# Performance work log

Measured on AMD Instinct MI355X. Metric: run time of the kernel, lower is better.

## Reference

```python
import jax, jax.numpy as jnp
import numpy as np

TEMPERATURE = 1.0
EPS = 1e-8


def setup_inputs() -> dict:
    key = jax.random.key(0)
    k1, k2, k3 = jax.random.split(key, 3)
    B, N = 32768, 32
    scores = jax.random.normal(k1, (B, N), dtype=jnp.float32)
    rankings = jax.random.randint(k2, (B, N), 0, 32, dtype=jnp.int64)
    mask = jax.random.randint(k3, (B, N), 0, 2) > 0
    return {"scores": scores, "rankings": rankings, "mask": mask}


def reference(scores, rankings, mask):
    # scores: [B, N] float, rankings: [B, N] int (0 => unranked), mask: [B, N] bool
    s = scores / TEMPERATURE
    valid = mask & (rankings > 0)                      # [B, N]

    ri = rankings[:, :, None]                          # [B, N, 1]
    rj = rankings[:, None, :]                          # [B, 1, N]
    # i==j implies ri==rj, so (ri != rj) also excludes the diagonal
    pair_valid = (valid[:, :, None] & valid[:, None, :] & (ri != rj))  # [B, N, N]

    p_ij = (ri < rj).astype(s.dtype)                   # target probability
    s_ij = jax.nn.sigmoid(s[:, :, None] - s[:, None, :])
    pair_loss = -p_ij * jnp.log(s_ij + EPS) - (1.0 - p_ij) * jnp.log(1.0 - s_ij + EPS)

    pv = pair_valid.astype(s.dtype)
    per_batch_sum = jnp.sum(pair_loss * pv, axis=(1, 2))     # [B]
    num_pairs = jnp.sum(pv, axis=(1, 2))                     # [B]

    has_pairs = num_pairs > 0
    per_batch_loss = jnp.where(has_pairs, per_batch_sum / jnp.maximum(num_pairs, 1.0), 0.0)
    n_batches = jnp.sum(has_pairs.astype(s.dtype))
    # reduction='mean' over batches that contributed pairs; 0.0 if none
    return jnp.where(n_batches > 0, jnp.sum(per_batch_loss) / jnp.maximum(n_batches, 1.0), 0.0)
```

## Files before the change

kernel.cpp:

```cpp
#include <hip/hip_runtime.h>

__global__ __launch_bounds__(256) void ranknet_partial_kernel(
    const float4* __restrict__ scores4,
    const int4*   __restrict__ rank4,
    const int4*   __restrict__ mask4,
    float2*       __restrict__ partials)
{
    const int gid  = blockIdx.x * 256 + threadIdx.x;
    const int lane = threadIdx.x & 63;
    const int wave = threadIdx.x >> 6;

    const float4 s4 = scores4[gid];
    const int4   r4 = rank4[gid];
    const int4   m4 = mask4[gid];

    const float L2E = 1.4426950408889634f;

    unsigned su[4];
    int      rj[4];
    float    rjnz[4];
    {
        const float sv[4] = {s4.x, s4.y, s4.z, s4.w};
        const int   rv[4] = {r4.x, r4.y, r4.z, r4.w};
        const int   mv[4] = {m4.x, m4.y, m4.z, m4.w};
        #pragma unroll
        for (int c = 0; c < 4; ++c) {
            const int rr = (mv[c] != 0 && rv[c] > 0) ? rv[c] : 0;
            su[c]   = (__float_as_uint(sv[c] * L2E) & ~31u) | (unsigned)rr;
            rj[c]   = rr;
            rjnz[c] = (rr != 0) ? 1.0f : 0.0f;
        }
    }

    float A = 0.0f;
    float P = 1.0f;
    float C = 0.0f;

    const bool low = ((lane & 7) < 4);

    #pragma unroll
    for (int t = 1; t <= 16; ++t) {
        #pragma unroll
        for (int c = 0; c < 4; ++c) {
            const int delta = (t + c) >> 2;
            const int gamma = (t + c) & 3;
            const int src   = (lane & ~7) | ((lane + delta) & 7);
            const unsigned pu = __shfl(su[gamma], src);

            const int   ri = (int)(pu & 31u);
            const float x  = __uint_as_float(pu) - __uint_as_float(su[c]);
            const float y  = (ri < rj[c]) ? -x : x;
            const float e  = __builtin_exp2f(-__builtin_fabsf(x));

            float validf = ((ri != 0) && (ri != rj[c])) ? rjnz[c] : 0.0f;
            if (t == 16) validf = low ? validf : 0.0f;

            A  = fmaf(validf, fmaxf(y, 0.0f), A);
            P *= fmaf(validf, e, 1.0f);
            C += validf;
        }
    }

    float v = A + __builtin_log2f(P);
    #pragma unroll
    for (int off = 1; off <= 4; off <<= 1) {
        v += __shfl_xor(v, off);
        C += __shfl_xor(C, off);
    }
    float pb  = (C > 0.0f) ? (v * 0.6931471805599453f) / C : 0.0f;
    float has = (C > 0.0f) ? 1.0f : 0.0f;

    #pragma unroll
    for (int off = 8; off <= 32; off <<= 1) {
        pb  += __shfl_xor(pb, off);
        has += __shfl_xor(has, off);
    }

    __shared__ float2 wpart[4];
    if (lane == 0) wpart[wave] = make_float2(pb, has);
    __syncthreads();
    if (threadIdx.x == 0) {
        float ps = 0.0f, pc = 0.0f;
        #pragma unroll
        for (int w2 = 0; w2 < 4; ++w2) { ps += wpart[w2].x; pc += wpart[w2].y; }
        partials[blockIdx.x] = make_float2(ps, pc);
    }
}

__global__ __launch_bounds__(256) void ranknet_finalize_kernel(
    const float2* __restrict__ partials, int n, float* __restrict__ out)
{
    float s = 0.0f, c = 0.0f;
    for (int i = threadIdx.x; i < n; i += 256) {
        const float2 p = partials[i];
        s += p.x;
        c += p.y;
    }
    #pragma unroll
    for (int off = 32; off > 0; off >>= 1) {
        s += __shfl_xor(s, off);
        c += __shfl_xor(c, off);
    }
    __shared__ float2 wsum[4];
    const int wave = threadIdx.x >> 6;
    const int lane = threadIdx.x & 63;
    if (lane == 0) wsum[wave] = make_float2(s, c);
    __syncthreads();
    if (threadIdx.x == 0) {
        float ts = 0.0f, tc = 0.0f;
        #pragma unroll
        for (int w = 0; w < 4; ++w) { ts += wsum[w].x; tc += wsum[w].y; }
        out[0] = (tc > 0.0f) ? (ts / tc) : 0.0f;
    }
}

extern "C" void kernel_launch(void* const* d_in, const int* in_sizes, int n_in,
                              void* d_out, int out_size, void* d_ws, size_t ws_size,
                              hipStream_t stream) {
    const float4* scores4 = (const float4*)d_in[0];
    const int4*   rank4   = (const int4*)d_in[1];
    const int4*   mask4   = (const int4*)d_in[2];
    float*        out     = (float*)d_out;

    const int total   = in_sizes[0];
    const int nblocks = total / 1024;

    float2* partials = (float2*)d_ws;

    ranknet_partial_kernel<<<nblocks, 256, 0, stream>>>(scores4, rank4, mask4, partials);
    ranknet_finalize_kernel<<<1, 256, 0, stream>>>(partials, nblocks, out);
}
```

Baseline: 15.86 us.

## Map each batch row to 16 lanes and use DPP row rotates

Each thread now holds 2 elements instead of 4, so one 32-element row is spread across a 16-lane DPP row. The per-pair exchanges then use row_ror DPP moves instead of ds_bpermute shuffles, and the intra-row reductions use DPP rotates as well. This doubles the thread count and grid size while cutting cross-lane latency, at the cost of narrower 8-byte loads and twice as many partials for the finalize kernel to sum.

```diff
diff --git a/kernel.cpp b/kernel.cpp
--- a/kernel.cpp
+++ b/kernel.cpp
@@ -1,80 +1,81 @@
 #include <hip/hip_runtime.h>
 
+template<int CTRL>
+__device__ __forceinline__ unsigned rowror(unsigned v) {
+    return (unsigned)__builtin_amdgcn_update_dpp(0, (int)v, CTRL, 0xF, 0xF, true);
+}
+
 __global__ __launch_bounds__(256) void ranknet_partial_kernel(
-    const float4* __restrict__ scores4,
-    const int4*   __restrict__ rank4,
-    const int4*   __restrict__ mask4,
+    const float2* __restrict__ scores2,
+    const int2*   __restrict__ rank2,
+    const int2*   __restrict__ mask2,
     float2*       __restrict__ partials)
 {
     const int gid  = blockIdx.x * 256 + threadIdx.x;
     const int lane = threadIdx.x & 63;
     const int wave = threadIdx.x >> 6;
 
-    const float4 s4 = scores4[gid];
-    const int4   r4 = rank4[gid];
-    const int4   m4 = mask4[gid];
+    const float2 s2 = scores2[gid];
+    const int2   r2 = rank2[gid];
+    const int2   m2 = mask2[gid];
 
     const float L2E = 1.4426950408889634f;
 
-    unsigned su[4];
-    int      rj[4];
-    float    rjnz[4];
-    {
-        const float sv[4] = {s4.x, s4.y, s4.z, s4.w};
-        const int   rv[4] = {r4.x, r4.y, r4.z, r4.w};
-        const int   mv[4] = {m4.x, m4.y, m4.z, m4.w};
-        #pragma unroll
-        for (int c = 0; c < 4; ++c) {
-            const int rr = (mv[c] != 0 && rv[c] > 0) ? rv[c] : 0;
-            su[c]   = (__float_as_uint(sv[c] * L2E) & ~31u) | (unsigned)rr;
-            rj[c]   = rr;
-            rjnz[c] = (rr != 0) ? 1.0f : 0.0f;
-        }
-    }
+    const int rr0 = (m2.x != 0 && r2.x > 0) ? r2.x : 0;
+    const int rr1 = (m2.y != 0 && r2.y > 0) ? r2.y : 0;
+    const unsigned su0 = (__float_as_uint(s2.x * L2E) & ~31u) | (unsigned)rr0;
+    const unsigned su1 = (__float_as_uint(s2.y * L2E) & ~31u) | (unsigned)rr1;
+    const float rjnz0 = (rr0 != 0) ? 1.0f : 0.0f;
+    const float rjnz1 = (rr1 != 0) ? 1.0f : 0.0f;
 
     float A = 0.0f;
     float P = 1.0f;
     float C = 0.0f;
 
-    const bool low = ((lane & 7) < 4);
+    auto slot = [&](unsigned lu, int rjc, float rjnzc, unsigned pu, float gate) {
+        const int   ri = (int)(pu & 31u);
+        const float x  = __uint_as_float(pu) - __uint_as_float(lu);
+        const float y  = (ri < rjc) ? -x : x;
+        const float e  = __builtin_exp2f(-__builtin_fabsf(x));
+        const float vf = ((ri != 0) && (ri != rjc)) ? (rjnzc * gate) : 0.0f;
+        A  = fmaf(vf, fmaxf(y, 0.0f), A);
+        P *= fmaf(vf, e, 1.0f);
+        C += vf;
+    };
 
-    #pragma unroll
-    for (int t = 1; t <= 16; ++t) {
-        #pragma unroll
-        for (int c = 0; c < 4; ++c) {
-            const int delta = (t + c) >> 2;
-            const int gamma = (t + c) & 3;
-            const int src   = (lane & ~7) | ((lane + delta) & 7);
-            const unsigned pu = __shfl(su[gamma], src);
+    slot(su0, rr0, rjnz0, su1, 1.0f);
 
-            const int   ri = (int)(pu & 31u);
-            const float x  = __uint_as_float(pu) - __uint_as_float(su[c]);
-            const float y  = (ri < rj[c]) ? -x : x;
-            const float e  = __builtin_exp2f(-__builtin_fabsf(x));
+#define DO_D(D, GATE) {                                   \
+        const unsigned pu0 = rowror<0x120 + (D)>(su0);    \
+        const unsigned pu1 = rowror<0x120 + (D)>(su1);    \
+        slot(su0, rr0, rjnz0, pu0, GATE);                 \
+        slot(su0, rr0, rjnz0, pu1, GATE);                 \
+        slot(su1, rr1, rjnz1, pu0, GATE);                 \
+        slot(su1, rr1, rjnz1, pu1, GATE); }
 
-            float validf = ((ri != 0) && (ri != rj[c])) ? rjnz[c] : 0.0f;
-            if (t == 16) validf = low ? validf : 0.0f;
-
-            A  = fmaf(validf, fmaxf(y, 0.0f), A);
-            P *= fmaf(validf, e, 1.0f);
-            C += validf;
-        }
-    }
+    DO_D(1, 1.0f)
+    DO_D(2, 1.0f)
+    DO_D(3, 1.0f)
+    DO_D(4, 1.0f)
+    DO_D(5, 1.0f)
+    DO_D(6, 1.0f)
+    DO_D(7, 1.0f)
+    const float g8 = ((lane & 15) < 8) ? 1.0f : 0.0f;
+    DO_D(8, g8)
+#undef DO_D
 
     float v = A + __builtin_log2f(P);
-    #pragma unroll
-    for (int off = 1; off <= 4; off <<= 1) {
-        v += __shfl_xor(v, off);
-        C += __shfl_xor(C, off);
-    }
+#define ROW_RED(D) {                                                        \
+        v += __uint_as_float(rowror<0x120 + (D)>(__float_as_uint(v)));      \
+        C += __uint_as_float(rowror<0x120 + (D)>(__float_as_uint(C))); }
+    ROW_RED(1) ROW_RED(2) ROW_RED(4) ROW_RED(8)
+#undef ROW_RED
+
     float pb  = (C > 0.0f) ? (v * 0.6931471805599453f) / C : 0.0f;
     float has = (C > 0.0f) ? 1.0f : 0.0f;
 
-    #pragma unroll
-    for (int off = 8; off <= 32; off <<= 1) {
-        pb  += __shfl_xor(pb, off);
-        has += __shfl_xor(has, off);
-    }
+    pb  += __shfl_xor(pb, 16);  has += __shfl_xor(has, 16);
+    pb  += __shfl_xor(pb, 32);  has += __shfl_xor(has, 32);
 
     __shared__ float2 wpart[4];
     if (lane == 0) wpart[wave] = make_float2(pb, has);
@@ -117,16 +118,16 @@
 extern "C" void kernel_launch(void* const* d_in, const int* in_sizes, int n_in,
                               void* d_out, int out_size, void* d_ws, size_t ws_size,
                               hipStream_t stream) {
-    const float4* scores4 = (const float4*)d_in[0];
-    const int4*   rank4   = (const int4*)d_in[1];
-    const int4*   mask4   = (const int4*)d_in[2];
+    const float2* scores2 = (const float2*)d_in[0];
+    const int2*   rank2   = (const int2*)d_in[1];
+    const int2*   mask2   = (const int2*)d_in[2];
     float*        out     = (float*)d_out;
 
     const int total   = in_sizes[0];
-    const int nblocks = total / 1024;
+    const int nblocks = total / 512;
 
     float2* partials = (float2*)d_ws;
 
-    ranknet_partial_kernel<<<nblocks, 256, 0, stream>>>(scores4, rank4, mask4, partials);
+    ranknet_partial_kernel<<<nblocks, 256, 0, stream>>>(scores2, rank2, mask2, partials);
     ranknet_finalize_kernel<<<1, 256, 0, stream>>>(partials, nblocks, out);
 }
```

Measured after the change: 17.07 us. 7.6% more time.
